# Performance work log

Hardware: AMD Instinct MI355X
Metric: run time of the kernel (lower is better)

The kernel has to match this reference:

```python
import jax, jax.numpy as jnp
import numpy as np

N, L, K, DROP = 4096, 128, 16, 1
LEFT = N - L * DROP  # 3968


def setup_inputs() -> dict:
    rng = np.random.RandomState(0)
    X = rng.randn(N, N).astype(np.float32)
    A = (X + X.T) / 2.0  # symmetric, like a graph Laplacian
    active = np.ones(N, dtype=bool)
    sel = np.zeros((L, K), dtype=np.int32)
    drp = np.zeros((L, DROP), dtype=np.int32)
    Os = np.zeros((L, K, K), dtype=np.float32)
    for l in range(L):
        cand = np.flatnonzero(active)
        idx = np.sort(rng.choice(cand, size=K, replace=False)).astype(np.int32)
        sel[l] = idx
        drp[l] = idx[:DROP]
        active[idx[:DROP]] = False
        Q, _ = np.linalg.qr(rng.randn(K, K))  # orthogonal init (eigvecs in original)
        Os[l] = Q.astype(np.float32)
    active_idx = np.flatnonzero(active).astype(np.int32)      # (LEFT,) sorted
    inactive_idx = np.flatnonzero(~active).astype(np.int32)   # (N-LEFT,) sorted
    return {
        'A': jnp.asarray(A),
        'Os': jnp.asarray(Os),
        'sel_idx': jnp.asarray(sel),
        'drop_idx': jnp.asarray(drp),
        'active_idx': jnp.asarray(active_idx),
        'inactive_idx': jnp.asarray(inactive_idx),
    }


def reference(A, Os, sel_idx, drop_idx, active_idx, inactive_idx):
    # U_l = I_N with the K x K orthogonal block O_l scattered at (sel, sel).
    # U A U^T therefore only changes K rows and K columns -> rank-K update,
    # identical math to the original dense torch.matmul(U, A) @ U.T.
    n = A.shape[0]
    right0 = jnp.eye(n, dtype=A.dtype)

    def step(carry, xs):
        A_l, right = carry
        O, sel, drp = xs
        A_l = A_l.at[sel, :].set(O @ A_l[sel, :])          # (U A): K rows change
        A_l = A_l.at[:, sel].set(A_l[:, sel] @ O.T)        # (. U^T): K cols change
        right = right.at[sel, :].set(O @ right[sel, :])    # right = U @ right
        wavelet = A_l[drp, :]                              # (drop, N)
        return (A_l, right), wavelet

    (A_L, right), wavelets = jax.lax.scan(step, (A, right0), (Os, sel_idx, drop_idx))
    # wavelets: (L, drop, N)

    active = jnp.zeros((n,), A.dtype).at[active_idx].set(1.0)
    # left_index = eye - diag(diag(outer)) + outer, with outer = active x active
    mask = jnp.eye(n, dtype=A.dtype) - jnp.diag(active) + jnp.outer(active, active)
    D = A_L * mask
    core_wavelets = A_L[active_idx, :]          # (LEFT, N), sorted active order
    mother_wavelets_2 = right[inactive_idx, :]  # (N-LEFT, N)
    father_wavelets_2 = right[active_idx, :]    # (LEFT, N)
    A_rec = right.T @ D @ right
    return A_rec, D, wavelets, core_wavelets, mother_wavelets_2, father_wavelets_2
```

## Files before the change

### kernel.cpp

```cpp
#include <hip/hip_runtime.h>
#include <hip/hip_bf16.h>
#include <stdint.h>

#define N 4096
#define TC 2048
#define LSTEPS 128
#define KSEL 16
#define NACT 3968
#define NIN 128

typedef __hip_bfloat16 bf16;
typedef __attribute__((ext_vector_type(8))) short short8;
typedef __attribute__((ext_vector_type(4))) float floatx4;

static __device__ __forceinline__ bf16 f2bf(float x) { return __float2bfloat16(x); }
static __device__ __forceinline__ float us2f(ushort u) { return __uint_as_float(((unsigned)u) << 16); }
static __device__ __forceinline__ ushort f2us(float x) { return __bfloat16_as_ushort(__float2bfloat16(x)); }

__global__ __launch_bounds__(1024) void touched_kernel(const int* __restrict__ sel,
                                                       const int* __restrict__ drp,
                                                       const int* __restrict__ act,
                                                       const int* __restrict__ inact,
                                                       int* __restrict__ tlist,
                                                       int* __restrict__ tpos,
                                                       int* __restrict__ tflag,
                                                       int* __restrict__ selc,
                                                       int* __restrict__ dposc,
                                                       int* __restrict__ flags,
                                                       int* __restrict__ rank) {
    __shared__ int flag[N];
    __shared__ int cpos[N];
    __shared__ int wsum[16];
    __shared__ int woff[16];
    __shared__ int s_tau;
    const int t = threadIdx.x;
#pragma unroll
    for (int k = 0; k < 4; k++) flag[t + 1024 * k] = 0;
    __syncthreads();
    flag[sel[t]] = 1;
    flag[sel[t + 1024]] = 1;
    __syncthreads();
    const int b0 = t * 4;
    const int a0 = flag[b0], a1 = flag[b0 + 1], a2 = flag[b0 + 2], a3 = flag[b0 + 3];
    const int s = a0 + a1 + a2 + a3;
    const int lane = t & 63, wv = t >> 6;
    int sc = s;
    for (int off = 1; off < 64; off <<= 1) {
        int o = __shfl_up(sc, off);
        if (lane >= off) sc += o;
    }
    if (lane == 63) wsum[wv] = sc;
    __syncthreads();
    if (t == 0) {
        int acc = 0;
        for (int i = 0; i < 16; i++) { woff[i] = acc; acc += wsum[i]; }
        s_tau = acc;
    }
    __syncthreads();
    const int tau = s_tau;
    const int need = TC - tau;
    int tp = woff[wv] + (sc - s);
    const int aa[4] = {a0, a1, a2, a3};
#pragma unroll
    for (int k = 0; k < 4; k++) {
        const int i = b0 + k;
        int ci;
        if (aa[k]) { ci = tp; tp++; }
        else {
            const int ur = i - tp;
            ci = (ur < need) ? (tau + ur) : -1;
        }
        cpos[i] = ci;
        tpos[i] = ci;
        tflag[i] = (ci >= 0) ? 1 : 0;
        if (ci >= 0) tlist[ci] = i;
    }
    __syncthreads();
    selc[t] = cpos[sel[t]];
    selc[t + 1024] = cpos[sel[t + 1024]];
    if (t < 128) dposc[t] = cpos[drp[t]];

#pragma unroll
    for (int k = 0; k < 4; k++) {
        const int i = b0 + k;
        int lo = 0, hi = NACT - 1, f = 0, r = -1;
        while (lo <= hi) {
            int mid = (lo + hi) >> 1, v = act[mid];
            if (v == i) { f = 1; r = mid; break; }
            if (v < i) lo = mid + 1; else hi = mid - 1;
        }
        if (!f) {
            lo = 0; hi = NIN - 1;
            while (lo <= hi) {
                int mid = (lo + hi) >> 1, v = inact[mid];
                if (v == i) { r = mid; break; }
                if (v < i) lo = mid + 1; else hi = mid - 1;
            }
        }
        flags[i] = f;
        rank[i] = r;
    }
}

__global__ __launch_bounds__(64) void rscanc_kernel(const float* __restrict__ Os,
                                                    const int* __restrict__ selc,
                                                    const int* __restrict__ dposc,
                                                    bf16* __restrict__ Rct,
                                                    bf16* __restrict__ Rd) {
    __shared__ float slab[TC * 4];
    const int t = threadIdx.x;
    const int cc = t & 3;
    const int a = t >> 2;
    const int c0 = blockIdx.x * 4;

    for (int r = t; r < TC * 4; r += 64) slab[r] = 0.0f;
    __syncthreads();
    if (t < 4) slab[(c0 + t) * 4 + t] = 1.0f;
    __syncthreads();

    int selr[16];
    float orow[16];
#pragma unroll
    for (int i = 0; i < 16; i++) selr[i] = selc[i];
#pragma unroll
    for (int i = 0; i < 16; i++) orow[i] = Os[a * 16 + i];

    for (int l = 0; l < LSTEPS; l++) {
        float p[16];
#pragma unroll
        for (int i = 0; i < 16; i++) p[i] = slab[selr[i] * 4 + cc];
#pragma unroll
        for (int i = 0; i < 16; i++) p[i] *= orow[i];
        const float s0 = (p[0] + p[1]) + (p[2] + p[3]);
        const float s1 = (p[4] + p[5]) + (p[6] + p[7]);
        const float s2 = (p[8] + p[9]) + (p[10] + p[11]);
        const float s3 = (p[12] + p[13]) + (p[14] + p[15]);
        const float v = (s0 + s1) + (s2 + s3);
        const int wrow = selr[a];
        int seln[16] = {0};
        float orown[16] = {0.f};
        if (l + 1 < LSTEPS) {
#pragma unroll
            for (int i = 0; i < 16; i++) seln[i] = selc[(l + 1) * 16 + i];
#pragma unroll
            for (int i = 0; i < 16; i++) orown[i] = Os[(l + 1) * 256 + a * 16 + i];
        }
        __syncthreads();
        slab[wrow * 4 + cc] = v;
        __syncthreads();
#pragma unroll
        for (int i = 0; i < 16; i++) { selr[i] = seln[i]; orow[i] = orown[i]; }
    }

    for (int ccw = 0; ccw < 4; ccw++) {
        bf16* dst = Rct + (size_t)(c0 + ccw) * TC;
        for (int r = t; r < TC; r += 64) dst[r] = f2bf(slab[r * 4 + ccw]);
    }
    for (int l = t; l < LSTEPS; l += 64) {
        const int rrow = dposc[l];
        ushort4 o;
        o.x = f2us(slab[rrow * 4 + 0]);
        o.y = f2us(slab[rrow * 4 + 1]);
        o.z = f2us(slab[rrow * 4 + 2]);
        o.w = f2us(slab[rrow * 4 + 3]);
        *(ushort4*)((ushort*)Rd + (size_t)l * TC + c0) = o;
    }
}

__global__ __launch_bounds__(256) void transB_kernel(const bf16* __restrict__ src,
                                                     bf16* __restrict__ dst,
                                                     int R, int C) {
    __shared__ ushort tile[64][65];
    const int t = threadIdx.x;
    const int bx = blockIdx.x, by = blockIdx.y;
    const int tr = t >> 4;
    const int tc = (t & 15) * 4;
#pragma unroll
    for (int k = 0; k < 4; k++) {
        int r = tr + 16 * k;
        const ushort* s = (const ushort*)src + (size_t)(by * 64 + r) * C + bx * 64 + tc;
        ushort4 v = *(const ushort4*)s;
        tile[r][tc + 0] = v.x; tile[r][tc + 1] = v.y;
        tile[r][tc + 2] = v.z; tile[r][tc + 3] = v.w;
    }
    __syncthreads();
#pragma unroll
    for (int k = 0; k < 4; k++) {
        int r = tr + 16 * k;
        ushort4 w;
        w.x = tile[tc + 0][r];
        w.y = tile[tc + 1][r];
        w.z = tile[tc + 2][r];
        w.w = tile[tc + 3][r];
        *(ushort4*)((ushort*)dst + (size_t)(bx * 64 + r) * R + by * 64 + tc) = w;
    }
}

__global__ __launch_bounds__(256) void transF_kernel(const float* __restrict__ src,
                                                     float* __restrict__ dst,
                                                     int R, int C) {
    __shared__ float tile[64][65];
    const int t = threadIdx.x;
    const int bx = blockIdx.x, by = blockIdx.y;
    const int tr = t >> 4;
    const int tc = (t & 15) * 4;
#pragma unroll
    for (int k = 0; k < 4; k++) {
        int r = tr + 16 * k;
        const float* s = src + (size_t)(by * 64 + r) * C + bx * 64 + tc;
        float4 v = *(const float4*)s;
        tile[r][tc + 0] = v.x; tile[r][tc + 1] = v.y;
        tile[r][tc + 2] = v.z; tile[r][tc + 3] = v.w;
    }
    __syncthreads();
#pragma unroll
    for (int k = 0; k < 4; k++) {
        int r = tr + 16 * k;
        float4 w;
        w.x = tile[tc + 0][r];
        w.y = tile[tc + 1][r];
        w.z = tile[tc + 2][r];
        w.w = tile[tc + 3][r];
        *(float4*)(dst + (size_t)(bx * 64 + r) * R + by * 64 + tc) = w;
    }
}

__global__ __launch_bounds__(256) void gatherAtT_kernel(const float* __restrict__ A,
                                                        const int* __restrict__ tlist,
                                                        bf16* __restrict__ AtT) {
    const int j = blockIdx.y;
    const int p0 = (blockIdx.x * 256 + threadIdx.x) * 4;
    const float* arow = A + (size_t)j * N;
    const int4 tl = *(const int4*)(tlist + p0);
    ushort4 o;
    o.x = f2us(arow[tl.x]); o.y = f2us(arow[tl.y]);
    o.z = f2us(arow[tl.z]); o.w = f2us(arow[tl.w]);
    *(ushort4*)((ushort*)AtT + (size_t)j * TC + p0) = o;
}

__global__ __launch_bounds__(256) void gatherRowsB_kernel(const bf16* __restrict__ src,
                                                          const int* __restrict__ tlist,
                                                          bf16* __restrict__ dst) {
    const int r = blockIdx.y;
    const int c0 = (blockIdx.x * 256 + threadIdx.x) * 4;
    ushort4 v = *(const ushort4*)((const ushort*)src + (size_t)tlist[r] * TC + c0);
    *(ushort4*)((ushort*)dst + (size_t)r * TC + c0) = v;
}

template <bool F32OUT>
__global__ __launch_bounds__(512) void gemmk_kernel(const bf16* __restrict__ Amat, int lda,
                                                    const bf16* __restrict__ Bt, int ldb,
                                                    void* __restrict__ Cv, int ldc, int K,
                                                    const int* __restrict__ rowmap) {
    __shared__ bf16 lds[4][(128 + 256) * 32];

    const int t = threadIdx.x;
    const int lane = t & 63;
    const int wave = t >> 6;
    const int wm = wave >> 2;
    const int wn = wave & 3;
    const int rowBase = blockIdx.y * 128;
    const int colBase = blockIdx.x * 256;

    const int sr = lane >> 2;
    const int sgo = (((lane & 3) ^ ((lane >> 3) & 3)) << 3);

    const int frow = lane & 15;
    const int fslot = (((lane >> 4) ^ ((lane >> 1) & 3)) << 4);
    const int aoff0 = (wm * 64 + frow) * 64 + fslot;
    const int boff0 = 128 * 64 + (wn * 64 + frow) * 64 + fslot;

    floatx4 acc[4][4] = {};

#define GK_STAGE_A(bufIdx, kk0)                                                                    \
    do {                                                                                           \
        const bf16* g_ = Amat + (size_t)(rowBase + wave * 16 + sr) * lda + (kk0) + sgo;            \
        char* l_ = (char*)&lds[bufIdx][0] + wave * 1024;                                           \
        __builtin_amdgcn_global_load_lds((const __attribute__((address_space(1))) void*)g_,        \
                                         (__attribute__((address_space(3))) void*)l_, 16, 0, 0);   \
    } while (0)
#define GK_STAGE_B(bufIdx, kk0)                                                                    \
    do {                                                                                           \
        const bf16* g0_ = Bt + (size_t)(colBase + wave * 32 + sr) * ldb + (kk0) + sgo;             \
        const bf16* g1_ = g0_ + (size_t)16 * ldb;                                                  \
        char* l0_ = (char*)&lds[bufIdx][128 * 32] + wave * 2048;                                   \
        __builtin_amdgcn_global_load_lds((const __attribute__((address_space(1))) void*)g0_,       \
                                         (__attribute__((address_space(3))) void*)l0_, 16, 0, 0);  \
        __builtin_amdgcn_global_load_lds((const __attribute__((address_space(1))) void*)g1_,       \
                                         (__attribute__((address_space(3))) void*)(l0_ + 1024),    \
                                         16, 0, 0);                                                \
    } while (0)

    const int NT = K >> 5;
#pragma unroll
    for (int p = 0; p < 3; p++) {
        GK_STAGE_A(p, p * 32);
        GK_STAGE_B(p, p * 32);
    }
    asm volatile("s_waitcnt vmcnt(6)" ::: "memory");
    __builtin_amdgcn_s_barrier();

    for (int tt = 0; tt < NT; tt++) {
        const int buf = tt & 3;
        const char* lA = (const char*)&lds[buf][0];
        const int nbuf = (tt + 3) & 3;
        const bool pf = (tt + 3) < NT;
        const int nk0 = (tt + 3) * 32;

        if (pf) GK_STAGE_A(nbuf, nk0);
        short8 af[4], bfv[4];
#pragma unroll
        for (int mi = 0; mi < 4; mi++) af[mi] = *(const short8*)(lA + aoff0 + mi * 1024);
#pragma unroll
        for (int ni = 0; ni < 2; ni++) bfv[ni] = *(const short8*)(lA + boff0 + ni * 1024);
        __builtin_amdgcn_s_barrier();
        asm volatile("s_waitcnt lgkmcnt(0)" ::: "memory");
        __builtin_amdgcn_s_setprio(1);
#pragma unroll
        for (int mi = 0; mi < 4; mi++)
#pragma unroll
            for (int ni = 0; ni < 2; ni++)
                acc[mi][ni] =
                    __builtin_amdgcn_mfma_f32_16x16x32_bf16(af[mi], bfv[ni], acc[mi][ni], 0, 0, 0);
        __builtin_amdgcn_s_setprio(0);
        __builtin_amdgcn_s_barrier();

        if (pf) GK_STAGE_B(nbuf, nk0);
#pragma unroll
        for (int ni = 2; ni < 4; ni++) bfv[ni] = *(const short8*)(lA + boff0 + ni * 1024);
        __builtin_amdgcn_s_barrier();
        asm volatile("s_waitcnt lgkmcnt(0)" ::: "memory");
        __builtin_amdgcn_s_setprio(1);
#pragma unroll
        for (int mi = 0; mi < 4; mi++)
#pragma unroll
            for (int ni = 2; ni < 4; ni++)
                acc[mi][ni] =
                    __builtin_amdgcn_mfma_f32_16x16x32_bf16(af[mi], bfv[ni], acc[mi][ni], 0, 0, 0);
        __builtin_amdgcn_s_setprio(0);
        asm volatile("s_waitcnt vmcnt(6)" ::: "memory");
        __builtin_amdgcn_s_barrier();
    }
#undef GK_STAGE_A
#undef GK_STAGE_B

    const int crow = (lane >> 4) * 4;
    const int ccol = lane & 15;
    const int rb = rowBase + wm * 64;
    const int cb = colBase + wn * 64;
#pragma unroll
    for (int mi = 0; mi < 4; mi++)
#pragma unroll
        for (int ni = 0; ni < 4; ni++)
#pragma unroll
            for (int r = 0; r < 4; r++) {
                const int gr0 = rb + mi * 16 + crow + r;
                const int gr = rowmap ? rowmap[gr0] : gr0;
                const int gc = cb + ni * 16 + ccol;
                if (F32OUT)
                    ((float*)Cv)[(size_t)gr * ldc + gc] = acc[mi][ni][r];
                else
                    ((bf16*)Cv)[(size_t)gr * ldc + gc] = f2bf(acc[mi][ni][r]);
            }
}

template <bool F32OUT>
__global__ __launch_bounds__(512) void gemm128_kernel(const bf16* __restrict__ Amat, int lda,
                                                      const bf16* __restrict__ Bt, int ldb,
                                                      void* __restrict__ Cv, int ldc, int K,
                                                      const int* __restrict__ rowmap) {
    __shared__ bf16 lds[4][(128 + 128) * 32];

    const int t = threadIdx.x;
    const int lane = t & 63;
    const int wave = t >> 6;
    const int wm = wave >> 1;
    const int wn = wave & 1;
    const int rowBase = blockIdx.y * 128;
    const int colBase = blockIdx.x * 128;

    const int sr = lane >> 2;
    const int sgo = (((lane & 3) ^ ((lane >> 3) & 3)) << 3);

    const int frow = lane & 15;
    const int fslot = (((lane >> 4) ^ ((lane >> 1) & 3)) << 4);
    const int aoff0 = (wm * 32 + frow) * 64 + fslot;
    const int boff0 = 128 * 64 + (wn * 64 + frow) * 64 + fslot;

    floatx4 acc[2][4] = {};

#define G1_STAGE_A(bufIdx, kk0)                                                                    \
    do {                                                                                           \
        const bf16* g_ = Amat + (size_t)(rowBase + wave * 16 + sr) * lda + (kk0) + sgo;            \
        char* l_ = (char*)&lds[bufIdx][0] + wave * 1024;                                           \
        __builtin_amdgcn_global_load_lds((const __attribute__((address_space(1))) void*)g_,        \
                                         (__attribute__((address_space(3))) void*)l_, 16, 0, 0);   \
    } while (0)
#define G1_STAGE_B(bufIdx, kk0)                                                                    \
    do {                                                                                           \
        const bf16* g_ = Bt + (size_t)(colBase + wave * 16 + sr) * ldb + (kk0) + sgo;              \
        char* l_ = (char*)&lds[bufIdx][128 * 32] + wave * 1024;                                    \
        __builtin_amdgcn_global_load_lds((const __attribute__((address_space(1))) void*)g_,        \
                                         (__attribute__((address_space(3))) void*)l_, 16, 0, 0);   \
    } while (0)

    const int NT = K >> 5;
#pragma unroll
    for (int p = 0; p < 3; p++) {
        G1_STAGE_A(p, p * 32);
        G1_STAGE_B(p, p * 32);
    }
    asm volatile("s_waitcnt vmcnt(4)" ::: "memory");
    __builtin_amdgcn_s_barrier();

    for (int tt = 0; tt < NT; tt++) {
        const int buf = tt & 3;
        const char* lA = (const char*)&lds[buf][0];
        const int nbuf = (tt + 3) & 3;
        const bool pf = (tt + 3) < NT;
        const int nk0 = (tt + 3) * 32;

        if (pf) G1_STAGE_A(nbuf, nk0);
        short8 af[2], bfv[4];
#pragma unroll
        for (int mi = 0; mi < 2; mi++) af[mi] = *(const short8*)(lA + aoff0 + mi * 1024);
#pragma unroll
        for (int ni = 0; ni < 2; ni++) bfv[ni] = *(const short8*)(lA + boff0 + ni * 1024);
        __builtin_amdgcn_s_barrier();
        asm volatile("s_waitcnt lgkmcnt(0)" ::: "memory");
        __builtin_amdgcn_s_setprio(1);
#pragma unroll
        for (int mi = 0; mi < 2; mi++)
#pragma unroll
            for (int ni = 0; ni < 2; ni++)
                acc[mi][ni] =
                    __builtin_amdgcn_mfma_f32_16x16x32_bf16(af[mi], bfv[ni], acc[mi][ni], 0, 0, 0);
        __builtin_amdgcn_s_setprio(0);
        __builtin_amdgcn_s_barrier();

        if (pf) G1_STAGE_B(nbuf, nk0);
#pragma unroll
        for (int ni = 2; ni < 4; ni++) bfv[ni] = *(const short8*)(lA + boff0 + ni * 1024);
        __builtin_amdgcn_s_barrier();
        asm volatile("s_waitcnt lgkmcnt(0)" ::: "memory");
        __builtin_amdgcn_s_setprio(1);
#pragma unroll
        for (int mi = 0; mi < 2; mi++)
#pragma unroll
            for (int ni = 2; ni < 4; ni++)
                acc[mi][ni] =
                    __builtin_amdgcn_mfma_f32_16x16x32_bf16(af[mi], bfv[ni], acc[mi][ni], 0, 0, 0);
        __builtin_amdgcn_s_setprio(0);
        asm volatile("s_waitcnt vmcnt(4)" ::: "memory");
        __builtin_amdgcn_s_barrier();
    }
#undef G1_STAGE_A
#undef G1_STAGE_B

    const int crow = (lane >> 4) * 4;
    const int ccol = lane & 15;
    const int rb = rowBase + wm * 32;
    const int cb = colBase + wn * 64;
#pragma unroll
    for (int mi = 0; mi < 2; mi++)
#pragma unroll
        for (int ni = 0; ni < 4; ni++)
#pragma unroll
            for (int r = 0; r < 4; r++) {
                const int gr0 = rb + mi * 16 + crow + r;
                const int gr = rowmap ? rowmap[gr0] : gr0;
                const int gc = cb + ni * 16 + ccol;
                if (F32OUT)
                    ((float*)Cv)[(size_t)gr * ldc + gc] = acc[mi][ni][r];
                else
                    ((bf16*)Cv)[(size_t)gr * ldc + gc] = f2bf(acc[mi][ni][r]);
            }
}

__global__ __launch_bounds__(256) void maskcore2_kernel(const float* __restrict__ A,
                                                        const bf16* __restrict__ Z,
                                                        const bf16* __restrict__ Zt,
                                                        const int* __restrict__ flags,
                                                        const int* __restrict__ rank,
                                                        const int* __restrict__ tflag,
                                                        const int* __restrict__ tpos,
                                                        float* __restrict__ Dout,
                                                        bf16* __restrict__ Dtc,
                                                        float* __restrict__ core) {
    const int i = blockIdx.y;
    const int j0 = (blockIdx.x * 256 + threadIdx.x) * 4;
    const int fi = flags[i];
    const int ri = rank[i];
    const int ti = tflag[i];
    const int pi = tpos[i];
    float4 vf;
    const int4 tf = *(const int4*)(tflag + j0);
    const int4 tp = *(const int4*)(tpos + j0);
    if (ti) {
        const ushort4 v16 = *(const ushort4*)((const ushort*)Z + (size_t)pi * N + j0);
        vf.x = us2f(v16.x); vf.y = us2f(v16.y); vf.z = us2f(v16.z); vf.w = us2f(v16.w);
    } else {
        vf = *(const float4*)(A + (size_t)i * N + j0);
        const ushort* zrow = (const ushort*)Zt + (size_t)i * TC;
        if (tf.x) vf.x = us2f(zrow[tp.x]);
        if (tf.y) vf.y = us2f(zrow[tp.y]);
        if (tf.z) vf.z = us2f(zrow[tp.z]);
        if (tf.w) vf.w = us2f(zrow[tp.w]);
    }
    if (fi) *(float4*)(core + (size_t)ri * N + j0) = vf;
    const int4 fj = *(const int4*)(flags + j0);
    const bool k0 = (i == j0 + 0) || (fi && fj.x);
    const bool k1 = (i == j0 + 1) || (fi && fj.y);
    const bool k2 = (i == j0 + 2) || (fi && fj.z);
    const bool k3 = (i == j0 + 3) || (fi && fj.w);
    float4 df;
    df.x = k0 ? vf.x : 0.0f; df.y = k1 ? vf.y : 0.0f;
    df.z = k2 ? vf.z : 0.0f; df.w = k3 ? vf.w : 0.0f;
    *(float4*)(Dout + (size_t)i * N + j0) = df;
    ushort* drow = (ushort*)Dtc + (size_t)i * TC;
    if (tf.x) drow[tp.x] = f2us(df.x);
    if (tf.y) drow[tp.y] = f2us(df.y);
    if (tf.z) drow[tp.z] = f2us(df.z);
    if (tf.w) drow[tp.w] = f2us(df.w);
}

__global__ __launch_bounds__(64) void wavelet_kernel(const bf16* __restrict__ Scw,
                                                     const float* __restrict__ Os,
                                                     const int* __restrict__ sel,
                                                     float* __restrict__ wout) {
    __shared__ float u[N];
    const int t = threadIdx.x;
    const int l = blockIdx.x;
    const ushort* src = (const ushort*)(Scw + (size_t)l * N);
    for (int j = t; j < N; j += 64) u[j] = us2f(src[j]);
    __syncthreads();
    for (int m = 0; m <= l; m++) {
        float v = 0.0f;
        int wrow = 0;
        if (t < 16) {
            float p[16];
#pragma unroll
            for (int i = 0; i < 16; i++) p[i] = u[sel[m * 16 + i]];
#pragma unroll
            for (int i = 0; i < 16; i++) p[i] *= Os[m * 256 + t * 16 + i];
            const float s0 = (p[0] + p[1]) + (p[2] + p[3]);
            const float s1 = (p[4] + p[5]) + (p[6] + p[7]);
            const float s2 = (p[8] + p[9]) + (p[10] + p[11]);
            const float s3 = (p[12] + p[13]) + (p[14] + p[15]);
            v = (s0 + s1) + (s2 + s3);
            wrow = sel[m * 16 + t];
        }
        __syncthreads();
        if (t < 16) u[wrow] = v;
        __syncthreads();
    }
    float* dst = wout + (size_t)l * N;
    for (int j = t; j < N; j += 64) dst[j] = u[j];
}

__global__ __launch_bounds__(256) void rowgatherR2_kernel(const bf16* __restrict__ Rc,
                                                          const int* __restrict__ flags,
                                                          const int* __restrict__ rank,
                                                          const int* __restrict__ tflag,
                                                          const int* __restrict__ tpos,
                                                          float* __restrict__ father,
                                                          float* __restrict__ mother) {
    const int i = blockIdx.x;
    const int t = threadIdx.x;
    float* dst = flags[i] ? (father + (size_t)rank[i] * N) : (mother + (size_t)rank[i] * N);
    const int ti = tflag[i];
    const ushort* rrow = (const ushort*)Rc + (size_t)(ti ? tpos[i] : 0) * TC;
    for (int it = 0; it < 4; it++) {
        const int j0 = (it * 256 + t) * 4;
        const int4 tf = *(const int4*)(tflag + j0);
        const int4 tp = *(const int4*)(tpos + j0);
        float4 o;
        o.x = tf.x ? (ti ? us2f(rrow[tp.x]) : 0.f) : ((j0 + 0 == i) ? 1.f : 0.f);
        o.y = tf.y ? (ti ? us2f(rrow[tp.y]) : 0.f) : ((j0 + 1 == i) ? 1.f : 0.f);
        o.z = tf.z ? (ti ? us2f(rrow[tp.z]) : 0.f) : ((j0 + 2 == i) ? 1.f : 0.f);
        o.w = tf.w ? (ti ? us2f(rrow[tp.w]) : 0.f) : ((j0 + 3 == i) ? 1.f : 0.f);
        *(float4*)(dst + j0) = o;
    }
}

__global__ __launch_bounds__(256) void arec_kernel(const float* __restrict__ W,
                                                   const float* __restrict__ Wt,
                                                   const float* __restrict__ D,
                                                   const int* __restrict__ tflag,
                                                   const int* __restrict__ tpos,
                                                   float* __restrict__ Arec) {
    const int i = blockIdx.y;
    const int j0 = (blockIdx.x * 256 + threadIdx.x) * 4;
    float4 o;
    if (tflag[i]) {
        o = *(const float4*)(W + (size_t)tpos[i] * N + j0);
    } else {
        o = *(const float4*)(D + (size_t)i * N + j0);
        const int4 tf = *(const int4*)(tflag + j0);
        const int4 tp = *(const int4*)(tpos + j0);
        const float* wrow = Wt + (size_t)i * TC;
        if (tf.x) o.x = wrow[tp.x];
        if (tf.y) o.y = wrow[tp.y];
        if (tf.z) o.z = wrow[tp.z];
        if (tf.w) o.w = wrow[tp.w];
    }
    *(float4*)(Arec + (size_t)i * N + j0) = o;
}

extern "C" void kernel_launch(void* const* d_in, const int* in_sizes, int n_in,
                              void* d_out, int out_size, void* d_ws, size_t ws_size,
                              hipStream_t stream) {
    const float* A = (const float*)d_in[0];
    const float* Os = (const float*)d_in[1];
    const int* sel = (const int*)d_in[2];
    const int* drp = (const int*)d_in[3];
    const int* act = (const int*)d_in[4];
    const int* inact = (const int*)d_in[5];

    float* out = (float*)d_out;
    float* out_Arec = out;
    float* out_D    = out + 16777216;
    float* out_wav  = out + 33554432;
    float* out_core = out + 34078720;
    float* out_moth = out + 50331648;
    float* out_fath = out + 50855936;

    char* ws = (char*)d_ws;
    const size_t KB = 1024;
    const size_t MB = 1024 * 1024;
    int* tlist = (int*)(ws + 0);
    int* tpos  = (int*)(ws + 64 * KB);
    int* tflag = (int*)(ws + 128 * KB);
    int* selc  = (int*)(ws + 192 * KB);
    int* flags = (int*)(ws + 256 * KB);
    int* rank  = (int*)(ws + 320 * KB);
    int* dposc = (int*)(ws + 384 * KB);
    bf16* Rd128 = (bf16*)(ws + 1 * MB);
    bf16* Scw   = (bf16*)(ws + 2 * MB);
    bf16* Rct   = (bf16*)(ws + 3 * MB);
    bf16* Rc    = (bf16*)(ws + 11 * MB);
    bf16* YT    = (bf16*)(ws + 19 * MB);
    bf16* Ac    = (bf16*)(ws + 35 * MB);
    bf16* Z     = (bf16*)(ws + 35 * MB);
    bf16* Zt    = (bf16*)(ws + 51 * MB);
    bf16* Dtc   = (bf16*)(ws + 67 * MB);
    bf16* Dc    = (bf16*)(ws + 83 * MB);
    float* W    = (float*)(ws + 19 * MB);
    float* Wt   = (float*)(ws + 51 * MB);

    touched_kernel<<<dim3(1), dim3(1024), 0, stream>>>(sel, drp, act, inact, tlist, tpos,
                                                       tflag, selc, dposc, flags, rank);
    gatherAtT_kernel<<<dim3(2, N), dim3(256), 0, stream>>>(A, tlist, YT);
    rscanc_kernel<<<dim3(TC / 4), dim3(64), 0, stream>>>(Os, selc, dposc, Rct, Rd128);
    transB_kernel<<<dim3(32, 32), dim3(256), 0, stream>>>(Rct, Rc, TC, TC);
    gemm128_kernel<false><<<dim3(32, 1), dim3(512), 0, stream>>>(Rd128, TC, YT, TC, Scw, N, TC,
                                                                 nullptr);
    wavelet_kernel<<<dim3(LSTEPS), dim3(64), 0, stream>>>(Scw, Os, sel, out_wav);
    gatherRowsB_kernel<<<dim3(2, TC), dim3(256), 0, stream>>>(YT, tlist, Ac);
    gemm128_kernel<false><<<dim3(16, 16), dim3(512), 0, stream>>>(Rc, TC, Ac, TC, YT, TC, TC,
                                                                  tlist);
    gemmk_kernel<false><<<dim3(16, 16), dim3(512), 0, stream>>>(Rc, TC, YT, TC, Z, N, TC, nullptr);
    transB_kernel<<<dim3(64, 32), dim3(256), 0, stream>>>(Z, Zt, TC, N);
    maskcore2_kernel<<<dim3(4, N), dim3(256), 0, stream>>>(A, Z, Zt, flags, rank, tflag, tpos,
                                                           out_D, Dtc, out_core);
    gatherRowsB_kernel<<<dim3(2, TC), dim3(256), 0, stream>>>(Dtc, tlist, Dc);
    gemm128_kernel<false><<<dim3(16, 16), dim3(512), 0, stream>>>(Rct, TC, Dc, TC, Dtc, TC, TC,
                                                                  tlist);
    gemmk_kernel<true><<<dim3(16, 16), dim3(512), 0, stream>>>(Rct, TC, Dtc, TC, W, N, TC,
                                                               nullptr);
    transF_kernel<<<dim3(64, 32), dim3(256), 0, stream>>>(W, Wt, TC, N);
    rowgatherR2_kernel<<<dim3(N), dim3(256), 0, stream>>>(Rc, flags, rank, tflag, tpos,
                                                          out_fath, out_moth);
    arec_kernel<<<dim3(4, N), dim3(256), 0, stream>>>(W, Wt, out_D, tflag, tpos, out_Arec);
}
```

Baseline: 720.8 us.

## Fuse gathers and transposes into GEMM epilogues via index maps

```diff
diff --git a/kernel.cpp b/kernel.cpp
--- a/kernel.cpp
+++ b/kernel.cpp
@@ -27,7 +27,9 @@
                                                        int* __restrict__ selc,
                                                        int* __restrict__ dposc,
                                                        int* __restrict__ flags,
-                                                       int* __restrict__ rank) {
+                                                       int* __restrict__ rank,
+                                                       int* __restrict__ zmap,
+                                                       int* __restrict__ offlist) {
     __shared__ int flag[N];
     __shared__ int cpos[N];
     __shared__ int wsum[16];
@@ -69,10 +71,12 @@
         else {
             const int ur = i - tp;
             ci = (ur < need) ? (tau + ur) : -1;
+            if (ci < 0) offlist[ur - need] = i;
         }
         cpos[i] = ci;
         tpos[i] = ci;
         tflag[i] = (ci >= 0) ? 1 : 0;
+        zmap[i] = (ci >= 0) ? (N + ci) : i;
         if (ci >= 0) tlist[ci] = i;
     }
     __syncthreads();
@@ -196,35 +200,6 @@
     }
 }
 
-__global__ __launch_bounds__(256) void transF_kernel(const float* __restrict__ src,
-                                                     float* __restrict__ dst,
-                                                     int R, int C) {
-    __shared__ float tile[64][65];
-    const int t = threadIdx.x;
-    const int bx = blockIdx.x, by = blockIdx.y;
-    const int tr = t >> 4;
-    const int tc = (t & 15) * 4;
-#pragma unroll
-    for (int k = 0; k < 4; k++) {
-        int r = tr + 16 * k;
-        const float* s = src + (size_t)(by * 64 + r) * C + bx * 64 + tc;
-        float4 v = *(const float4*)s;
-        tile[r][tc + 0] = v.x; tile[r][tc + 1] = v.y;
-        tile[r][tc + 2] = v.z; tile[r][tc + 3] = v.w;
-    }
-    __syncthreads();
-#pragma unroll
-    for (int k = 0; k < 4; k++) {
-        int r = tr + 16 * k;
-        float4 w;
-        w.x = tile[tc + 0][r];
-        w.y = tile[tc + 1][r];
-        w.z = tile[tc + 2][r];
-        w.w = tile[tc + 3][r];
-        *(float4*)(dst + (size_t)(bx * 64 + r) * R + by * 64 + tc) = w;
-    }
-}
-
 __global__ __launch_bounds__(256) void gatherAtT_kernel(const float* __restrict__ A,
                                                         const int* __restrict__ tlist,
                                                         bf16* __restrict__ AtT) {
@@ -238,20 +213,13 @@
     *(ushort4*)((ushort*)AtT + (size_t)j * TC + p0) = o;
 }
 
-__global__ __launch_bounds__(256) void gatherRowsB_kernel(const bf16* __restrict__ src,
-                                                          const int* __restrict__ tlist,
-                                                          bf16* __restrict__ dst) {
-    const int r = blockIdx.y;
-    const int c0 = (blockIdx.x * 256 + threadIdx.x) * 4;
-    ushort4 v = *(const ushort4*)((const ushort*)src + (size_t)tlist[r] * TC + c0);
-    *(ushort4*)((ushort*)dst + (size_t)r * TC + c0) = v;
-}
-
 template <bool F32OUT>
 __global__ __launch_bounds__(512) void gemmk_kernel(const bf16* __restrict__ Amat, int lda,
                                                     const bf16* __restrict__ Bt, int ldb,
                                                     void* __restrict__ Cv, int ldc, int K,
-                                                    const int* __restrict__ rowmap) {
+                                                    const int* __restrict__ rowmap,
+                                                    const int* __restrict__ bmap,
+                                                    void* __restrict__ Tt, int ldt) {
     __shared__ bf16 lds[4][(128 + 256) * 32];
 
     const int t = threadIdx.x;
@@ -264,6 +232,10 @@
 
     const int sr = lane >> 2;
     const int sgo = (((lane & 3) ^ ((lane >> 3) & 3)) << 3);
+
+    const int bR = colBase + wave * 32 + sr;
+    const int bIdx0 = bmap ? bmap[bR] : bR;
+    const int bIdx1 = bmap ? bmap[bR + 16] : (bR + 16);
 
     const int frow = lane & 15;
     const int fslot = (((lane >> 4) ^ ((lane >> 1) & 3)) << 4);
@@ -281,8 +253,8 @@
     } while (0)
 #define GK_STAGE_B(bufIdx, kk0)                                                                    \
     do {                                                                                           \
-        const bf16* g0_ = Bt + (size_t)(colBase + wave * 32 + sr) * ldb + (kk0) + sgo;             \
-        const bf16* g1_ = g0_ + (size_t)16 * ldb;                                                  \
+        const bf16* g0_ = Bt + (size_t)bIdx0 * ldb + (kk0) + sgo;                                  \
+        const bf16* g1_ = Bt + (size_t)bIdx1 * ldb + (kk0) + sgo;                                  \
         char* l0_ = (char*)&lds[bufIdx][128 * 32] + wave * 2048;                                   \
         __builtin_amdgcn_global_load_lds((const __attribute__((address_space(1))) void*)g0_,       \
                                          (__attribute__((address_space(3))) void*)l0_, 16, 0, 0);  \
@@ -346,29 +318,43 @@
 
     const int crow = (lane >> 4) * 4;
     const int ccol = lane & 15;
-    const int rb = rowBase + wm * 64;
+    const int rbc = rowBase + wm * 64;
     const int cb = colBase + wn * 64;
 #pragma unroll
     for (int mi = 0; mi < 4; mi++)
 #pragma unroll
-        for (int ni = 0; ni < 4; ni++)
+        for (int ni = 0; ni < 4; ni++) {
+            const int grc = rbc + mi * 16 + crow;
+            const int gc = cb + ni * 16 + ccol;
 #pragma unroll
             for (int r = 0; r < 4; r++) {
-                const int gr0 = rb + mi * 16 + crow + r;
-                const int gr = rowmap ? rowmap[gr0] : gr0;
-                const int gc = cb + ni * 16 + ccol;
+                const int gr = rowmap ? rowmap[grc + r] : (grc + r);
                 if (F32OUT)
                     ((float*)Cv)[(size_t)gr * ldc + gc] = acc[mi][ni][r];
                 else
                     ((bf16*)Cv)[(size_t)gr * ldc + gc] = f2bf(acc[mi][ni][r]);
             }
+            if (Tt) {
+                if (F32OUT) {
+                    float4 w;
+                    w.x = acc[mi][ni][0]; w.y = acc[mi][ni][1];
+                    w.z = acc[mi][ni][2]; w.w = acc[mi][ni][3];
+                    *(float4*)((float*)Tt + (size_t)gc * ldt + grc) = w;
+                } else {
+                    ushort4 w;
+                    w.x = f2us(acc[mi][ni][0]); w.y = f2us(acc[mi][ni][1]);
+                    w.z = f2us(acc[mi][ni][2]); w.w = f2us(acc[mi][ni][3]);
+                    *(ushort4*)((ushort*)Tt + (size_t)gc * ldt + grc) = w;
+                }
+            }
+        }
 }
 
 template <bool F32OUT>
 __global__ __launch_bounds__(512) void gemm128_kernel(const bf16* __restrict__ Amat, int lda,
                                                       const bf16* __restrict__ Bt, int ldb,
                                                       void* __restrict__ Cv, int ldc, int K,
-                                                      const int* __restrict__ rowmap) {
+                                                      const int* __restrict__ bmap) {
     __shared__ bf16 lds[4][(128 + 128) * 32];
 
     const int t = threadIdx.x;
@@ -381,6 +367,9 @@
 
     const int sr = lane >> 2;
     const int sgo = (((lane & 3) ^ ((lane >> 3) & 3)) << 3);
+
+    const int bR = colBase + wave * 16 + sr;
+    const int bIdx = bmap ? bmap[bR] : bR;
 
     const int frow = lane & 15;
     const int fslot = (((lane >> 4) ^ ((lane >> 1) & 3)) << 4);
@@ -398,7 +387,7 @@
     } while (0)
 #define G1_STAGE_B(bufIdx, kk0)                                                                    \
     do {                                                                                           \
-        const bf16* g_ = Bt + (size_t)(colBase + wave * 16 + sr) * ldb + (kk0) + sgo;              \
+        const bf16* g_ = Bt + (size_t)bIdx * ldb + (kk0) + sgo;                                    \
         char* l_ = (char*)&lds[bufIdx][128 * 32] + wave * 1024;                                    \
         __builtin_amdgcn_global_load_lds((const __attribute__((address_space(1))) void*)g_,        \
                                          (__attribute__((address_space(3))) void*)l_, 16, 0, 0);   \
@@ -467,8 +456,7 @@
         for (int ni = 0; ni < 4; ni++)
 #pragma unroll
             for (int r = 0; r < 4; r++) {
-                const int gr0 = rb + mi * 16 + crow + r;
-                const int gr = rowmap ? rowmap[gr0] : gr0;
+                const int gr = rb + mi * 16 + crow + r;
                 const int gc = cb + ni * 16 + ccol;
                 if (F32OUT)
                     ((float*)Cv)[(size_t)gr * ldc + gc] = acc[mi][ni][r];
@@ -531,27 +519,19 @@
     __shared__ float u[N];
     const int t = threadIdx.x;
     const int l = blockIdx.x;
+    const int a = t >> 2, q = t & 3;
     const ushort* src = (const ushort*)(Scw + (size_t)l * N);
     for (int j = t; j < N; j += 64) u[j] = us2f(src[j]);
     __syncthreads();
     for (int m = 0; m <= l; m++) {
-        float v = 0.0f;
-        int wrow = 0;
-        if (t < 16) {
-            float p[16];
-#pragma unroll
-            for (int i = 0; i < 16; i++) p[i] = u[sel[m * 16 + i]];
-#pragma unroll
-            for (int i = 0; i < 16; i++) p[i] *= Os[m * 256 + t * 16 + i];
-            const float s0 = (p[0] + p[1]) + (p[2] + p[3]);
-            const float s1 = (p[4] + p[5]) + (p[6] + p[7]);
-            const float s2 = (p[8] + p[9]) + (p[10] + p[11]);
-            const float s3 = (p[12] + p[13]) + (p[14] + p[15]);
-            v = (s0 + s1) + (s2 + s3);
-            wrow = sel[m * 16 + t];
-        }
+        const int4 si = *(const int4*)(sel + m * 16 + q * 4);
+        const float4 ov = *(const float4*)(Os + m * 256 + a * 16 + q * 4);
+        float pp = ov.x * u[si.x] + ov.y * u[si.y] + ov.z * u[si.z] + ov.w * u[si.w];
+        pp += __shfl_xor(pp, 1);
+        pp += __shfl_xor(pp, 2);
+        const int wrow = sel[m * 16 + a];
         __syncthreads();
-        if (t < 16) u[wrow] = v;
+        if (q == 0) u[wrow] = pp;
         __syncthreads();
     }
     float* dst = wout + (size_t)l * N;
@@ -583,27 +563,22 @@
     }
 }
 
-__global__ __launch_bounds__(256) void arec_kernel(const float* __restrict__ W,
-                                                   const float* __restrict__ Wt,
-                                                   const float* __restrict__ D,
-                                                   const int* __restrict__ tflag,
-                                                   const int* __restrict__ tpos,
-                                                   float* __restrict__ Arec) {
-    const int i = blockIdx.y;
+__global__ __launch_bounds__(256) void arecoff_kernel(const float* __restrict__ D,
+                                                      const float* __restrict__ Wt,
+                                                      const int* __restrict__ offlist,
+                                                      const int* __restrict__ tflag,
+                                                      const int* __restrict__ tpos,
+                                                      float* __restrict__ Arec) {
+    const int i = offlist[blockIdx.y];
     const int j0 = (blockIdx.x * 256 + threadIdx.x) * 4;
-    float4 o;
-    if (tflag[i]) {
-        o = *(const float4*)(W + (size_t)tpos[i] * N + j0);
-    } else {
-        o = *(const float4*)(D + (size_t)i * N + j0);
-        const int4 tf = *(const int4*)(tflag + j0);
-        const int4 tp = *(const int4*)(tpos + j0);
-        const float* wrow = Wt + (size_t)i * TC;
-        if (tf.x) o.x = wrow[tp.x];
-        if (tf.y) o.y = wrow[tp.y];
-        if (tf.z) o.z = wrow[tp.z];
-        if (tf.w) o.w = wrow[tp.w];
-    }
+    float4 o = *(const float4*)(D + (size_t)i * N + j0);
+    const int4 tf = *(const int4*)(tflag + j0);
+    const int4 tp = *(const int4*)(tpos + j0);
+    const float* wrow = Wt + (size_t)i * TC;
+    if (tf.x) o.x = wrow[tp.x];
+    if (tf.y) o.y = wrow[tp.y];
+    if (tf.z) o.z = wrow[tp.z];
+    if (tf.w) o.w = wrow[tp.w];
     *(float4*)(Arec + (size_t)i * N + j0) = o;
 }
 
@@ -628,48 +603,45 @@
     char* ws = (char*)d_ws;
     const size_t KB = 1024;
     const size_t MB = 1024 * 1024;
-    int* tlist = (int*)(ws + 0);
-    int* tpos  = (int*)(ws + 64 * KB);
-    int* tflag = (int*)(ws + 128 * KB);
-    int* selc  = (int*)(ws + 192 * KB);
-    int* flags = (int*)(ws + 256 * KB);
-    int* rank  = (int*)(ws + 320 * KB);
-    int* dposc = (int*)(ws + 384 * KB);
+    int* tlist   = (int*)(ws + 0);
+    int* tpos    = (int*)(ws + 64 * KB);
+    int* tflag   = (int*)(ws + 128 * KB);
+    int* selc    = (int*)(ws + 192 * KB);
+    int* flags   = (int*)(ws + 256 * KB);
+    int* rank    = (int*)(ws + 320 * KB);
+    int* dposc   = (int*)(ws + 384 * KB);
+    int* zmap    = (int*)(ws + 448 * KB);
+    int* offlist = (int*)(ws + 512 * KB);
     bf16* Rd128 = (bf16*)(ws + 1 * MB);
     bf16* Scw   = (bf16*)(ws + 2 * MB);
     bf16* Rct   = (bf16*)(ws + 3 * MB);
     bf16* Rc    = (bf16*)(ws + 11 * MB);
-    bf16* YT    = (bf16*)(ws + 19 * MB);
-    bf16* Ac    = (bf16*)(ws + 35 * MB);
-    bf16* Z     = (bf16*)(ws + 35 * MB);
-    bf16* Zt    = (bf16*)(ws + 51 * MB);
-    bf16* Dtc   = (bf16*)(ws + 67 * MB);
-    bf16* Dc    = (bf16*)(ws + 83 * MB);
-    float* W    = (float*)(ws + 19 * MB);
-    float* Wt   = (float*)(ws + 51 * MB);
-
-    touched_kernel<<<dim3(1), dim3(1024), 0, stream>>>(sel, drp, act, inact, tlist, tpos,
-                                                       tflag, selc, dposc, flags, rank);
-    gatherAtT_kernel<<<dim3(2, N), dim3(256), 0, stream>>>(A, tlist, YT);
+    bf16* Breg  = (bf16*)(ws + 19 * MB);
+    bf16* Yc    = Breg + (size_t)N * TC;
+    bf16* Z     = (bf16*)(ws + 43 * MB);
+    bf16* Zt    = (bf16*)(ws + 59 * MB);
+    float* Wt   = (float*)(ws + 43 * MB);
+
+    touched_kernel<<<dim3(1), dim3(1024), 0, stream>>>(sel, drp, act, inact, tlist, tpos, tflag,
+                                                       selc, dposc, flags, rank, zmap, offlist);
+    gatherAtT_kernel<<<dim3(2, N), dim3(256), 0, stream>>>(A, tlist, Breg);
     rscanc_kernel<<<dim3(TC / 4), dim3(64), 0, stream>>>(Os, selc, dposc, Rct, Rd128);
     transB_kernel<<<dim3(32, 32), dim3(256), 0, stream>>>(Rct, Rc, TC, TC);
-    gemm128_kernel<false><<<dim3(32, 1), dim3(512), 0, stream>>>(Rd128, TC, YT, TC, Scw, N, TC,
+    gemm128_kernel<false><<<dim3(32, 1), dim3(512), 0, stream>>>(Rd128, TC, Breg, TC, Scw, N, TC,
                                                                  nullptr);
     wavelet_kernel<<<dim3(LSTEPS), dim3(64), 0, stream>>>(Scw, Os, sel, out_wav);
-    gatherRowsB_kernel<<<dim3(2, TC), dim3(256), 0, stream>>>(YT, tlist, Ac);
-    gemm128_kernel<false><<<dim3(16, 16), dim3(512), 0, stream>>>(Rc, TC, Ac, TC, YT, TC, TC,
+    gemm128_kernel<false><<<dim3(16, 16), dim3(512), 0, stream>>>(Rc, TC, Breg, TC, Yc, TC, TC,
                                                                   tlist);
-    gemmk_kernel<false><<<dim3(16, 16), dim3(512), 0, stream>>>(Rc, TC, YT, TC, Z, N, TC, nullptr);
-    transB_kernel<<<dim3(64, 32), dim3(256), 0, stream>>>(Z, Zt, TC, N);
+    gemmk_kernel<false><<<dim3(16, 16), dim3(512), 0, stream>>>(Rc, TC, Breg, TC, Z, N, TC,
+                                                                nullptr, zmap, Zt, TC);
     maskcore2_kernel<<<dim3(4, N), dim3(256), 0, stream>>>(A, Z, Zt, flags, rank, tflag, tpos,
-                                                           out_D, Dtc, out_core);
-    gatherRowsB_kernel<<<dim3(2, TC), dim3(256), 0, stream>>>(Dtc, tlist, Dc);
-    gemm128_kernel<false><<<dim3(16, 16), dim3(512), 0, stream>>>(Rct, TC, Dc, TC, Dtc, TC, TC,
+                                                           out_D, Breg, out_core);
+    gemm128_kernel<false><<<dim3(16, 16), dim3(512), 0, stream>>>(Rct, TC, Breg, TC, Yc, TC, TC,
                                                                   tlist);
-    gemmk_kernel<true><<<dim3(16, 16), dim3(512), 0, stream>>>(Rct, TC, Dtc, TC, W, N, TC,
-                                                               nullptr);
-    transF_kernel<<<dim3(64, 32), dim3(256), 0, stream>>>(W, Wt, TC, N);
+    gemmk_kernel<true><<<dim3(16, 16), dim3(512), 0, stream>>>(Rct, TC, Breg, TC, out_Arec, N, TC,
+                                                               tlist, zmap, Wt, TC);
+    arecoff_kernel<<<dim3(4, N - TC), dim3(256), 0, stream>>>(out_D, Wt, offlist, tflag, tpos,
+                                                              out_Arec);
     rowgatherR2_kernel<<<dim3(N), dim3(256), 0, stream>>>(Rc, flags, rank, tflag, tpos,
                                                           out_fath, out_moth);
-    arec_kernel<<<dim3(4, N), dim3(256), 0, stream>>>(W, Wt, out_D, tflag, tpos, out_Arec);
-}
+}
```

Result: faster. 705.9 us (-2.1%).
